# Performance work log

Measured on AMD Instinct MI355X. Metric: run time of the kernel, lower is better.

## Reference

```python
import jax, jax.numpy as jnp
import numpy as np

B, H, S, E = 16384, 16, 1, 64
N_OTHERS = 4


def setup_inputs() -> dict:
    key = jax.random.key(0)
    ks = jax.random.split(key, N_OTHERS + 2)
    inp = {f"others_{i}": jax.random.normal(ks[i], (B, H, S, E), dtype=jnp.float32)
           for i in range(N_OTHERS)}
    inp["main"] = jax.random.normal(ks[N_OTHERS], (B, H, S, E), dtype=jnp.float32)
    inp["W"] = jax.random.normal(ks[N_OTHERS + 1], (E, E), dtype=jnp.float32) * (1.0 / np.sqrt(E))
    return inp


def reference(others_0, others_1, others_2, others_3, main, W):
    # mean over the 'others' modalities: (B, H, 1, E)
    mean = (others_0 + others_1 + others_2 + others_3) / 4.0
    m = jnp.squeeze(mean, 2)        # (B, H, E)
    main_sq = jnp.squeeze(main, 2)  # (B, H, E)
    # bilinear score: mean @ W @ main^T -> (B, H, H)
    score = jnp.einsum('bhe,ef,bgf->bhg', m, W, main_sq)
    attn = jax.nn.softmax(score, axis=-1)      # (B, H, H)
    context = jnp.einsum('bhg,bge->bhe', attn, main_sq)  # (B, H, E)
    return context, attn
```

## Files before the change

### kernel.cpp

```cpp
#include <hip/hip_runtime.h>

#define NBATCH 16384
#define H 16
#define E 64

#define LGKM0 do { asm volatile("s_waitcnt lgkmcnt(0)" ::: "memory"); \
                   __builtin_amdgcn_sched_barrier(0); } while (0)

__global__ __launch_bounds__(64, 3) void ovo_kernel(
    const float* __restrict__ o0, const float* __restrict__ o1,
    const float* __restrict__ o2, const float* __restrict__ o3,
    const float* __restrict__ mn, const float* __restrict__ W,
    float* __restrict__ ctx_out, float* __restrict__ attn_out)
{
    __shared__ float sMeanP[H][68];
    __shared__ float sMainP[H][68];
    __shared__ float sMW[H][68];

    const int l = threadIdx.x;
    const size_t base = (size_t)blockIdx.x * (H * E);

    float4 ra[4], rb[4], rc[4], rd[4], rv[4];
#pragma unroll
    for (int k = 0; k < 4; ++k) {
        const int off = k * 256 + l * 4;
        ra[k] = *(const float4*)(o0 + base + off);
        rb[k] = *(const float4*)(o1 + base + off);
        rc[k] = *(const float4*)(o2 + base + off);
        rd[k] = *(const float4*)(o3 + base + off);
        rv[k] = *(const float4*)(mn + base + off);
    }

#pragma unroll
    for (int k = 0; k < 4; ++k) {
        const int flat = k * 256 + l * 4;
        const int h = flat >> 6, e = flat & 63;
        float4 m4;
        m4.x = (ra[k].x + rb[k].x + rc[k].x + rd[k].x) * 0.25f;
        m4.y = (ra[k].y + rb[k].y + rc[k].y + rd[k].y) * 0.25f;
        m4.z = (ra[k].z + rb[k].z + rc[k].z + rd[k].z) * 0.25f;
        m4.w = (ra[k].w + rb[k].w + rc[k].w + rd[k].w) * 0.25f;
        *(float4*)&sMeanP[h][e] = m4;
        *(float4*)&sMainP[h][e] = rv[k];
    }
    LGKM0;

    {
        const int ht = l >> 4, ft = l & 15;
        const int h0 = ht * 4, f0 = ft * 4;
        float acc[4][4] = {{0.f}};
#pragma unroll
        for (int e0 = 0; e0 < 64; e0 += 4) {
            float4 mrow[4], wrow[4];
#pragma unroll
            for (int i = 0; i < 4; ++i) mrow[i] = *(const float4*)&sMeanP[h0 + i][e0];
#pragma unroll
            for (int j = 0; j < 4; ++j) wrow[j] = *(const float4*)&W[(e0 + j) * 64 + f0];
#pragma unroll
            for (int i = 0; i < 4; ++i) {
                const float* mr = (const float*)&mrow[i];
#pragma unroll
                for (int ee = 0; ee < 4; ++ee) {
                    const float* wr = (const float*)&wrow[ee];
#pragma unroll
                    for (int j = 0; j < 4; ++j)
                        acc[i][j] = fmaf(mr[ee], wr[j], acc[i][j]);
                }
            }
        }
#pragma unroll
        for (int i = 0; i < 4; ++i)
            *(float4*)&sMW[h0 + i][f0] =
                make_float4(acc[i][0], acc[i][1], acc[i][2], acc[i][3]);
    }
    LGKM0;

    {
        const int hp = l >> 3, gp = l & 7;
        const int h0 = hp * 2, g0 = gp * 2;
        float sc00 = 0.f, sc01 = 0.f, sc10 = 0.f, sc11 = 0.f;
#pragma unroll
        for (int f0 = 0; f0 < 64; f0 += 4) {
            float4 a0 = *(const float4*)&sMW[h0][f0];
            float4 a1 = *(const float4*)&sMW[h0 + 1][f0];
            float4 b0 = *(const float4*)&sMainP[g0][f0];
            float4 b1 = *(const float4*)&sMainP[g0 + 1][f0];
            const float* pa0 = (const float*)&a0;
            const float* pa1 = (const float*)&a1;
            const float* pb0 = (const float*)&b0;
            const float* pb1 = (const float*)&b1;
#pragma unroll
            for (int q = 0; q < 4; ++q) {
                sc00 = fmaf(pa0[q], pb0[q], sc00);
                sc01 = fmaf(pa0[q], pb1[q], sc01);
                sc10 = fmaf(pa1[q], pb0[q], sc10);
                sc11 = fmaf(pa1[q], pb1[q], sc11);
            }
        }
        *(float2*)&sMeanP[h0][g0]     = make_float2(sc00, sc01);
        *(float2*)&sMeanP[h0 + 1][g0] = make_float2(sc10, sc11);
    }
    LGKM0;

    {
        const int h = l >> 2, q = l & 3;
        float4 sc = *(const float4*)&sMeanP[h][q * 4];
        float mx = fmaxf(fmaxf(sc.x, sc.y), fmaxf(sc.z, sc.w));
        mx = fmaxf(mx, __shfl_xor(mx, 1));
        mx = fmaxf(mx, __shfl_xor(mx, 2));
        float e0 = __expf(sc.x - mx), e1 = __expf(sc.y - mx);
        float e2 = __expf(sc.z - mx), e3 = __expf(sc.w - mx);
        float sum = (e0 + e1) + (e2 + e3);
        sum += __shfl_xor(sum, 1);
        sum += __shfl_xor(sum, 2);
        const float inv = 1.0f / sum;
        float4 a4 = make_float4(e0 * inv, e1 * inv, e2 * inv, e3 * inv);
        *(float4*)&sMeanP[h][q * 4] = a4;
        *(float4*)(attn_out + (size_t)blockIdx.x * (H * H) + l * 4) = a4;
    }
    LGKM0;

    {
        const int ht = l >> 4, et = l & 15;
        const int h0 = ht * 4, e0c = et * 4;
        float acc[4][4] = {{0.f}};
#pragma unroll
        for (int g0 = 0; g0 < 16; g0 += 4) {
            float4 bv[4];
#pragma unroll
            for (int gg = 0; gg < 4; ++gg)
                bv[gg] = *(const float4*)&sMainP[g0 + gg][e0c];
#pragma unroll
            for (int i = 0; i < 4; ++i) {
                float4 av = *(const float4*)&sMeanP[h0 + i][g0];
                const float* pa = (const float*)&av;
#pragma unroll
                for (int gg = 0; gg < 4; ++gg) {
                    const float* pb = (const float*)&bv[gg];
#pragma unroll
                    for (int j = 0; j < 4; ++j)
                        acc[i][j] = fmaf(pa[gg], pb[j], acc[i][j]);
                }
            }
        }
        float* cp = ctx_out + base;
#pragma unroll
        for (int i = 0; i < 4; ++i)
            *(float4*)(cp + (h0 + i) * 64 + e0c) =
                make_float4(acc[i][0], acc[i][1], acc[i][2], acc[i][3]);
    }
}

extern "C" void kernel_launch(void* const* d_in, const int* in_sizes, int n_in,
                              void* d_out, int out_size, void* d_ws, size_t ws_size,
                              hipStream_t stream) {
    const float* o0 = (const float*)d_in[0];
    const float* o1 = (const float*)d_in[1];
    const float* o2 = (const float*)d_in[2];
    const float* o3 = (const float*)d_in[3];
    const float* mn = (const float*)d_in[4];
    const float* W  = (const float*)d_in[5];
    float* ctx  = (float*)d_out;
    float* attn = ctx + (size_t)NBATCH * H * E;
    hipLaunchKernelGGL(ovo_kernel, dim3(NBATCH), dim3(64), 0, stream,
                       o0, o1, o2, o3, mn, W, ctx, attn);
}
```

Measured before the change: 95.81 us.

## Alias shared buffers, keep scores in registers, raise occupancy hint

The shared-memory footprint drops from three padded 16x68 arrays to two by reusing one buffer for the mean, then M·W, then the transposed attention matrix. The score stage is remapped so each thread computes the four scores its softmax lane needs and keeps them in registers, which removes one LDS round trip. The launch-bounds occupancy hint rises from 3 to 5 so more waves can be resident to hide global load latency. The costs are tighter register budgets that may cause spills, an extra wait before the in-place overwrite, and scalar strided LDS reads of attention in the context stage.

New measurement: 112.2 us. 1.17x slower.

```diff
diff --git a/kernel.cpp b/kernel.cpp
--- a/kernel.cpp
+++ b/kernel.cpp
@@ -7,15 +7,14 @@
 #define LGKM0 do { asm volatile("s_waitcnt lgkmcnt(0)" ::: "memory"); \
                    __builtin_amdgcn_sched_barrier(0); } while (0)
 
-__global__ __launch_bounds__(64, 3) void ovo_kernel(
+__global__ __launch_bounds__(64, 5) void ovo_kernel(
     const float* __restrict__ o0, const float* __restrict__ o1,
     const float* __restrict__ o2, const float* __restrict__ o3,
     const float* __restrict__ mn, const float* __restrict__ W,
     float* __restrict__ ctx_out, float* __restrict__ attn_out)
 {
-    __shared__ float sMeanP[H][68];
-    __shared__ float sMainP[H][68];
-    __shared__ float sMW[H][68];
+    __shared__ float sA[H * 68];
+    __shared__ float sMain[H * 68];
 
     const int l = threadIdx.x;
     const size_t base = (size_t)blockIdx.x * (H * E);
@@ -40,8 +39,8 @@
         m4.y = (ra[k].y + rb[k].y + rc[k].y + rd[k].y) * 0.25f;
         m4.z = (ra[k].z + rb[k].z + rc[k].z + rd[k].z) * 0.25f;
         m4.w = (ra[k].w + rb[k].w + rc[k].w + rd[k].w) * 0.25f;
-        *(float4*)&sMeanP[h][e] = m4;
-        *(float4*)&sMainP[h][e] = rv[k];
+        *(float4*)&sA[h * 68 + e] = m4;
+        *(float4*)&sMain[h * 68 + e] = rv[k];
     }
     LGKM0;
 
@@ -53,7 +52,7 @@
         for (int e0 = 0; e0 < 64; e0 += 4) {
             float4 mrow[4], wrow[4];
 #pragma unroll
-            for (int i = 0; i < 4; ++i) mrow[i] = *(const float4*)&sMeanP[h0 + i][e0];
+            for (int i = 0; i < 4; ++i) mrow[i] = *(const float4*)&sA[(h0 + i) * 68 + e0];
 #pragma unroll
             for (int j = 0; j < 4; ++j) wrow[j] = *(const float4*)&W[(e0 + j) * 64 + f0];
 #pragma unroll
@@ -68,55 +67,51 @@
                 }
             }
         }
+        LGKM0;
 #pragma unroll
         for (int i = 0; i < 4; ++i)
-            *(float4*)&sMW[h0 + i][f0] =
+            *(float4*)&sA[(h0 + i) * 68 + f0] =
                 make_float4(acc[i][0], acc[i][1], acc[i][2], acc[i][3]);
     }
     LGKM0;
 
-    {
-        const int hp = l >> 3, gp = l & 7;
-        const int h0 = hp * 2, g0 = gp * 2;
-        float sc00 = 0.f, sc01 = 0.f, sc10 = 0.f, sc11 = 0.f;
+    const int hp = l >> 2, gp = l & 3;
+    const int g0 = gp * 4;
+    float sc[4] = {0.f, 0.f, 0.f, 0.f};
 #pragma unroll
-        for (int f0 = 0; f0 < 64; f0 += 4) {
-            float4 a0 = *(const float4*)&sMW[h0][f0];
-            float4 a1 = *(const float4*)&sMW[h0 + 1][f0];
-            float4 b0 = *(const float4*)&sMainP[g0][f0];
-            float4 b1 = *(const float4*)&sMainP[g0 + 1][f0];
-            const float* pa0 = (const float*)&a0;
-            const float* pa1 = (const float*)&a1;
-            const float* pb0 = (const float*)&b0;
-            const float* pb1 = (const float*)&b1;
+    for (int f0 = 0; f0 < 64; f0 += 4) {
+        float4 a0 = *(const float4*)&sA[hp * 68 + f0];
+        const float* pa = (const float*)&a0;
+        float4 b[4];
 #pragma unroll
-            for (int q = 0; q < 4; ++q) {
-                sc00 = fmaf(pa0[q], pb0[q], sc00);
-                sc01 = fmaf(pa0[q], pb1[q], sc01);
-                sc10 = fmaf(pa1[q], pb0[q], sc10);
-                sc11 = fmaf(pa1[q], pb1[q], sc11);
-            }
+        for (int j = 0; j < 4; ++j)
+            b[j] = *(const float4*)&sMain[(g0 + j) * 68 + f0];
+#pragma unroll
+        for (int j = 0; j < 4; ++j) {
+            const float* pb = (const float*)&b[j];
+#pragma unroll
+            for (int q = 0; q < 4; ++q)
+                sc[j] = fmaf(pa[q], pb[q], sc[j]);
         }
-        *(float2*)&sMeanP[h0][g0]     = make_float2(sc00, sc01);
-        *(float2*)&sMeanP[h0 + 1][g0] = make_float2(sc10, sc11);
     }
     LGKM0;
 
     {
-        const int h = l >> 2, q = l & 3;
-        float4 sc = *(const float4*)&sMeanP[h][q * 4];
-        float mx = fmaxf(fmaxf(sc.x, sc.y), fmaxf(sc.z, sc.w));
+        float mx = fmaxf(fmaxf(sc[0], sc[1]), fmaxf(sc[2], sc[3]));
         mx = fmaxf(mx, __shfl_xor(mx, 1));
         mx = fmaxf(mx, __shfl_xor(mx, 2));
-        float e0 = __expf(sc.x - mx), e1 = __expf(sc.y - mx);
-        float e2 = __expf(sc.z - mx), e3 = __expf(sc.w - mx);
+        float e0 = __expf(sc[0] - mx), e1 = __expf(sc[1] - mx);
+        float e2 = __expf(sc[2] - mx), e3 = __expf(sc[3] - mx);
         float sum = (e0 + e1) + (e2 + e3);
         sum += __shfl_xor(sum, 1);
         sum += __shfl_xor(sum, 2);
         const float inv = 1.0f / sum;
         float4 a4 = make_float4(e0 * inv, e1 * inv, e2 * inv, e3 * inv);
-        *(float4*)&sMeanP[h][q * 4] = a4;
         *(float4*)(attn_out + (size_t)blockIdx.x * (H * H) + l * 4) = a4;
+        const float* pa4 = (const float*)&a4;
+#pragma unroll
+        for (int j = 0; j < 4; ++j)
+            sA[(g0 + j) * 20 + hp] = pa4[j];
     }
     LGKM0;
 
@@ -125,23 +120,18 @@
         const int h0 = ht * 4, e0c = et * 4;
         float acc[4][4] = {{0.f}};
 #pragma unroll
-        for (int g0 = 0; g0 < 16; g0 += 4) {
-            float4 bv[4];
+        for (int g = 0; g < 16; ++g) {
+            float4 bv = *(const float4*)&sMain[g * 68 + e0c];
+            const float* pb = (const float*)&bv;
+            float av[4];
 #pragma unroll
-            for (int gg = 0; gg < 4; ++gg)
-                bv[gg] = *(const float4*)&sMainP[g0 + gg][e0c];
+            for (int i = 0; i < 4; ++i)
+                av[i] = sA[g * 20 + h0 + i];
 #pragma unroll
-            for (int i = 0; i < 4; ++i) {
-                float4 av = *(const float4*)&sMeanP[h0 + i][g0];
-                const float* pa = (const float*)&av;
+            for (int i = 0; i < 4; ++i)
 #pragma unroll
-                for (int gg = 0; gg < 4; ++gg) {
-                    const float* pb = (const float*)&bv[gg];
-#pragma unroll
-                    for (int j = 0; j < 4; ++j)
-                        acc[i][j] = fmaf(pa[gg], pb[j], acc[i][j]);
-                }
-            }
+                for (int j = 0; j < 4; ++j)
+                    acc[i][j] = fmaf(av[i], pb[j], acc[i][j]);
         }
         float* cp = ctx_out + base;
 #pragma unroll
```
